# Kernel tuning notes

Hardware: AMD Instinct MI355X
Metric: run time of the kernel (lower is better)

The kernel has to match this reference:

```python
import jax, jax.numpy as jnp
import numpy as np
from jax import lax

EPS = 1e-5
DN = ('NCDHW', 'OIDHW', 'NCDHW')


def _instance_norm(x, w, b):
    # normalize over spatial dims per (batch, channel); biased variance like torch
    mu = jnp.mean(x, axis=(2, 3, 4), keepdims=True)
    var = jnp.mean((x - mu) ** 2, axis=(2, 3, 4), keepdims=True)
    xn = (x - mu) * lax.rsqrt(var + EPS)
    return xn * w[None, :, None, None, None] + b[None, :, None, None, None]


def _conv1x1(x, w, b):
    # w: [Cout, Cin]
    y = jnp.einsum('bcdhw,oc->bodhw', x, w)
    return y + b[None, :, None, None, None]


def _dwconv3(x, w, b):
    # depthwise 3x3x3, padding 1; w: [C, 1, 3, 3, 3]
    y = lax.conv_general_dilated(x, w, (1, 1, 1), 'SAME',
                                 dimension_numbers=DN,
                                 feature_group_count=w.shape[0])
    return y + b[None, :, None, None, None]


def setup_inputs() -> dict:
    key = jax.random.key(0)
    ks = jax.random.split(key, 8)
    C, half = 64, 32
    B, D, H, W = 1, 96, 96, 96
    s1 = 1.0 / np.sqrt(C)          # fan_in of 1x1 conv
    s3 = 1.0 / np.sqrt(27.0)       # fan_in of depthwise 3x3x3
    return {
        'x': jax.random.normal(ks[0], (B, C, D, H, W), jnp.float32),
        'norm_w': jnp.ones((C,), jnp.float32),
        'norm_b': jnp.zeros((C,), jnp.float32),
        'in_proj_w': jax.random.normal(ks[1], (C, C), jnp.float32) * s1,
        'in_proj_b': jnp.zeros((C,), jnp.float32),
        'conv_ssm_w': jax.random.normal(ks[2], (half, 1, 3, 3, 3), jnp.float32) * s3,
        'conv_ssm_b': jnp.zeros((half,), jnp.float32),
        'mamba_w': jax.random.normal(ks[3], (half, 1, 3, 3, 3), jnp.float32) * s3,
        'mamba_b': jnp.zeros((half,), jnp.float32),
        'conv_sym_w': jax.random.normal(ks[4], (half, 1, 3, 3, 3), jnp.float32) * s3,
        'conv_sym_b': jnp.zeros((half,), jnp.float32),
        'out_proj_w': jax.random.normal(ks[5], (C, C), jnp.float32) * s1,
        'out_proj_b': jnp.zeros((C,), jnp.float32),
    }


def reference(x, norm_w, norm_b, in_proj_w, in_proj_b,
              conv_ssm_w, conv_ssm_b, mamba_w, mamba_b,
              conv_sym_w, conv_sym_b, out_proj_w, out_proj_b):
    residual = x
    xp = _conv1x1(_instance_norm(x, norm_w, norm_b), in_proj_w, in_proj_b)
    half = xp.shape[1] // 2
    x1, x2 = xp[:, :half], xp[:, half:]
    # SSM branch (TriDirectionalMamba fallback = depthwise conv3)
    x1 = _dwconv3(jax.nn.silu(_dwconv3(x1, conv_ssm_w, conv_ssm_b)), mamba_w, mamba_b)
    # symmetric conv branch
    x2 = jax.nn.silu(_dwconv3(x2, conv_sym_w, conv_sym_b))
    y = _conv1x1(jnp.concatenate([x1, x2], axis=1), out_proj_w, out_proj_b)
    return y + residual
```

## Files before the change

kernel.cpp:

```cpp
#include <hip/hip_runtime.h>

typedef unsigned short u16;
typedef unsigned int u32;
typedef short bf16x8 __attribute__((ext_vector_type(8)));
typedef float f32x16 __attribute__((ext_vector_type(16)));
typedef u16 u16x8 __attribute__((ext_vector_type(8)));

#define DIM 96
#define PLANE (DIM*DIM)
#define S 884736
#define C 64
#define HALF 32
#define PARTS 16
#define EPS 1e-5f
#define DSPLIT 4
#define DCHUNK (DIM/DSPLIT)

#define MFMA32(a,b,c) __builtin_amdgcn_mfma_f32_32x32x16_bf16(a,b,c,0,0,0)

__device__ __forceinline__ u16 f2bf(float f) {
  u32 u = __builtin_bit_cast(u32, f);
  return (u16)((u + 0x7FFFu + ((u >> 16) & 1u)) >> 16);
}
__device__ __forceinline__ float bf2f(u16 h) {
  return __builtin_bit_cast(float, (u32)h << 16);
}
__device__ __forceinline__ u32 cvt_pk_bf16(float lo, float hi) {
  u32 r;
  asm("v_cvt_pk_bf16_f32 %0, %1, %2" : "=v"(r) : "v"(lo), "v"(hi));
  return r;
}
__device__ __forceinline__ float silu(float v) { return v / (1.f + __expf(-v)); }
__device__ __forceinline__ u16x8 zero8() {
  u16x8 z;
  #pragma unroll
  for (int i = 0; i < 8; ++i) z[i] = 0;
  return z;
}

__global__ __launch_bounds__(256) void k1_stats(const float* __restrict__ x,
                                                u16* __restrict__ xb,
                                                float* __restrict__ psum,
                                                float* __restrict__ psq) {
  const int bid = blockIdx.x;
  const int ch = bid / PARTS, part = bid % PARTS;
  const int chunk = S / PARTS;
  const size_t base = (size_t)ch * S + (size_t)part * chunk;
  const float4* p = (const float4*)(x + base);
  ushort4* xb4 = (ushort4*)(xb + base);
  const int n4 = chunk / 4;
  float s = 0.f, q = 0.f;
  for (int i = threadIdx.x; i < n4; i += 256) {
    float4 v = p[i];
    s += (v.x + v.y) + (v.z + v.w);
    q += (v.x * v.x + v.y * v.y) + (v.z * v.z + v.w * v.w);
    union { u32 u[2]; ushort4 v4; } o;
    o.u[0] = cvt_pk_bf16(v.x, v.y);
    o.u[1] = cvt_pk_bf16(v.z, v.w);
    xb4[i] = o.v4;
  }
  #pragma unroll
  for (int off = 32; off > 0; off >>= 1) {
    s += __shfl_down(s, off);
    q += __shfl_down(q, off);
  }
  __shared__ float ls[4], lq[4];
  const int wid = threadIdx.x >> 6, lane = threadIdx.x & 63;
  if (lane == 0) { ls[wid] = s; lq[wid] = q; }
  __syncthreads();
  if (threadIdx.x == 0) {
    psum[bid] = (ls[0] + ls[1]) + (ls[2] + ls[3]);
    psq[bid]  = (lq[0] + lq[1]) + (lq[2] + lq[3]);
  }
}

__global__ __launch_bounds__(64) void k1b_prep(const float* __restrict__ psum,
    const float* __restrict__ psq,
    const float* __restrict__ norm_w, const float* __restrict__ norm_b,
    const float* __restrict__ in_w, const float* __restrict__ in_b,
    const float* __restrict__ out_w,
    u16* __restrict__ Wp, float* __restrict__ biasp, u16* __restrict__ Wo) {
  __shared__ float a_s[C], b2_s[C];
  const int t = threadIdx.x;
  float s = 0.f, q = 0.f;
  for (int i = 0; i < PARTS; ++i) { s += psum[t * PARTS + i]; q += psq[t * PARTS + i]; }
  const float inv = 1.f / (float)S;
  const float mu = s * inv;
  const float var = q * inv - mu * mu;
  const float rsig = rsqrtf(var + EPS);
  const float a = norm_w[t] * rsig;
  const float b2 = norm_b[t] - mu * a;
  a_s[t] = a; b2_s[t] = b2;
  __syncthreads();
  float bp = in_b[t];
  for (int c = 0; c < C; ++c) {
    const float w = in_w[t * C + c];
    Wp[t * C + c] = f2bf(w * a_s[c]);
    bp += b2_s[c] * w;
    Wo[t * C + c] = f2bf(out_w[t * C + c]);
  }
  biasp[t] = bp;
}

__global__ __launch_bounds__(256) void k2_mfma(const u16* __restrict__ xb,
    const u16* __restrict__ Wp, const float* __restrict__ biasp,
    u16* __restrict__ xp) {
  const int lane = threadIdx.x & 63, wid = threadIdx.x >> 6;
  const int n = lane & 31, hf = lane >> 5;
  const int v0 = blockIdx.x * 256 + wid * 64;
  bf16x8 A[2][4];
  #pragma unroll
  for (int t = 0; t < 2; ++t)
    #pragma unroll
    for (int s = 0; s < 4; ++s)
      A[t][s] = *(const bf16x8*)(Wp + (t * 32 + n) * C + s * 16 + hf * 8);

  f32x16 accE[2], accO[2];
  #pragma unroll
  for (int t = 0; t < 2; ++t)
    #pragma unroll
    for (int r = 0; r < 16; ++r) {
      const float b = biasp[t * 32 + (r & 3) + 8 * (r >> 2) + 4 * hf];
      accE[t][r] = b; accO[t][r] = b;
    }

  #pragma unroll
  for (int s = 0; s < 4; ++s) {
    union { u16 u[8]; bf16x8 v; } BE, BO;
    #pragma unroll
    for (int j = 0; j < 8; ++j) {
      const u32 xv = *(const u32*)(xb + (size_t)(s * 16 + hf * 8 + j) * S + v0 + 2 * n);
      BE.u[j] = (u16)(xv & 0xFFFFu); BO.u[j] = (u16)(xv >> 16);
    }
    #pragma unroll
    for (int t = 0; t < 2; ++t) {
      accE[t] = MFMA32(A[t][s], BE.v, accE[t]);
      accO[t] = MFMA32(A[t][s], BO.v, accO[t]);
    }
  }
  #pragma unroll
  for (int t = 0; t < 2; ++t)
    #pragma unroll
    for (int r = 0; r < 16; ++r) {
      const int o = t * 32 + (r & 3) + 8 * (r >> 2) + 4 * hf;
      *(u32*)(xp + (size_t)o * S + v0 + 2 * n) = cvt_pk_bf16(accE[t][r], accO[t][r]);
    }
}

__device__ __forceinline__ void fma_row8(float* __restrict__ a,
    const float* __restrict__ r, float t0, float t1, float t2) {
  #pragma unroll
  for (int i = 0; i < 8; ++i) a[i] += t0 * r[i] + t1 * r[i + 1] + t2 * r[i + 2];
}

template<bool SILU>
__global__ __launch_bounds__(192) void dwconv(const u16* __restrict__ srcA,
    const float* __restrict__ kwA, const float* __restrict__ bA,
    u16* __restrict__ dstA,
    const float* __restrict__ kwB, const float* __restrict__ bB,
    u16* __restrict__ dstB) {
  const int c = blockIdx.z;
  const u16* src = srcA + (size_t)c * S;
  u16* dst; const float* kwp; float bias;
  if (c < HALF) { dst = dstA + (size_t)c * S;          kwp = kwA + c * 27;          bias = bA[c]; }
  else          { dst = dstB + (size_t)(c - HALF) * S; kwp = kwB + (c - HALF) * 27; bias = bB[c - HALF]; }
  float kw[27];
  #pragma unroll
  for (int i = 0; i < 27; ++i) kw[i] = kwp[i];

  const int w8 = threadIdx.x * 8;
  const int h  = blockIdx.x * 16 + threadIdx.y;
  const bool hm = h > 0, hp = h < DIM - 1;
  const bool wlo = w8 > 0, whi = w8 < DIM - 8;
  const int d0 = blockIdx.y * DCHUNK;

  u16x8 Qm[3]; u16 Qlo[3], Qhi[3];
  u16x8 Pm[3]; u16 Plo[3], Phi[3];
  float r0[10], r1[10], r2[10];
  float A[8], B[8], o8[8];

  #define RAWLOAD(M, LO, HI, PPTR) { \
    const u16* _p = (PPTR); \
    if (hm) { M[0] = *(const u16x8*)(_p - DIM); LO[0] = wlo ? _p[-DIM - 1] : (u16)0; HI[0] = whi ? _p[-DIM + 8] : (u16)0; } \
    else    { M[0] = zero8(); LO[0] = 0; HI[0] = 0; } \
    {         M[1] = *(const u16x8*)(_p);       LO[1] = wlo ? _p[-1]       : (u16)0; HI[1] = whi ? _p[8]        : (u16)0; } \
    if (hp) { M[2] = *(const u16x8*)(_p + DIM); LO[2] = wlo ? _p[DIM - 1]  : (u16)0; HI[2] = whi ? _p[DIM + 8]  : (u16)0; } \
    else    { M[2] = zero8(); LO[2] = 0; HI[2] = 0; } }

  #define CONVERT(M, LO, HI) { \
    r0[0] = bf2f(LO[0]); r1[0] = bf2f(LO[1]); r2[0] = bf2f(LO[2]); \
    _Pragma("unroll") \
    for (int i = 0; i < 8; ++i) { \
      r0[1 + i] = bf2f(M[0][i]); r1[1 + i] = bf2f(M[1][i]); r2[1 + i] = bf2f(M[2][i]); } \
    r0[9] = bf2f(HI[0]); r1[9] = bf2f(HI[1]); r2[9] = bf2f(HI[2]); }

  #define ZROWS() { \
    _Pragma("unroll") \
    for (int i = 0; i < 10; ++i) { r0[i] = 0.f; r1[i] = 0.f; r2[i] = 0.f; } }

  #define CBLK(ACC, K0) \
    fma_row8(ACC, r0, kw[(K0) + 0], kw[(K0) + 1], kw[(K0) + 2]); \
    fma_row8(ACC, r1, kw[(K0) + 3], kw[(K0) + 4], kw[(K0) + 5]); \
    fma_row8(ACC, r2, kw[(K0) + 6], kw[(K0) + 7], kw[(K0) + 8]);

  #define COMPUTE_STORE() { \
    _Pragma("unroll") \
    for (int i = 0; i < 8; ++i) o8[i] = A[i]; \
    CBLK(o8, 18); \
    _Pragma("unroll") \
    for (int i = 0; i < 8; ++i) A[i] = B[i]; \
    CBLK(A, 9); \
    _Pragma("unroll") \
    for (int i = 0; i < 8; ++i) B[i] = bias; \
    CBLK(B, 0); \
    if (SILU) { \
      _Pragma("unroll") \
      for (int i = 0; i < 8; ++i) o8[i] = silu(o8[i]); \
    } \
    union { u32 u[4]; u16x8 v; } _o; \
    _Pragma("unroll") \
    for (int i = 0; i < 4; ++i) _o.u[i] = cvt_pk_bf16(o8[2 * i], o8[2 * i + 1]); \
    *(u16x8*)db = _o.v; \
    db += PLANE; }

  const u16* pb0 = src + h * DIM + w8;

  if (d0 > 0) {
    RAWLOAD(Qm, Qlo, Qhi, pb0 + (size_t)(d0 - 1) * PLANE); CONVERT(Qm, Qlo, Qhi);
    #pragma unroll
    for (int i = 0; i < 8; ++i) B[i] = bias;
    CBLK(B, 0);
  } else {
    #pragma unroll
    for (int i = 0; i < 8; ++i) B[i] = bias;
  }
  RAWLOAD(Qm, Qlo, Qhi, pb0 + (size_t)d0 * PLANE); CONVERT(Qm, Qlo, Qhi);
  #pragma unroll
  for (int i = 0; i < 8; ++i) { A[i] = B[i]; B[i] = bias; }
  CBLK(A, 9);
  CBLK(B, 0);
  RAWLOAD(Qm, Qlo, Qhi, pb0 + (size_t)(d0 + 1) * PLANE);
  RAWLOAD(Pm, Plo, Phi, pb0 + (size_t)(d0 + 2) * PLANE);
  const u16* pA = pb0 + (size_t)(d0 + 3) * PLANE;
  const u16* pB = pA + PLANE;
  u16* db = dst + (size_t)d0 * PLANE + h * DIM + w8;

  #pragma unroll 1
  for (int d = d0; d < d0 + DCHUNK; d += 2) {
    CONVERT(Qm, Qlo, Qhi);
    if (d + 3 < DIM) { RAWLOAD(Qm, Qlo, Qhi, pA); }
    pA += 2 * PLANE;
    COMPUTE_STORE();
    if (d + 2 < DIM) { CONVERT(Pm, Plo, Phi); } else { ZROWS(); }
    if (d + 4 < DIM) { RAWLOAD(Pm, Plo, Phi, pB); }
    pB += 2 * PLANE;
    COMPUTE_STORE();
  }
  #undef COMPUTE_STORE
  #undef CBLK
  #undef ZROWS
  #undef CONVERT
  #undef RAWLOAD
}

__global__ __launch_bounds__(256) void k4b_mfma(const u16* __restrict__ z_lo,
    const u16* __restrict__ z_hi, const u16* __restrict__ xb,
    const u16* __restrict__ Wo, const float* __restrict__ ob,
    float* __restrict__ out) {
  const int lane = threadIdx.x & 63, wid = threadIdx.x >> 6;
  const int n = lane & 31, hf = lane >> 5;
  const int v0 = blockIdx.x * 256 + wid * 64;
  bf16x8 A[2][4];
  #pragma unroll
  for (int t = 0; t < 2; ++t)
    #pragma unroll
    for (int s = 0; s < 4; ++s)
      A[t][s] = *(const bf16x8*)(Wo + (t * 32 + n) * C + s * 16 + hf * 8);

  f32x16 accE[2], accO[2];
  #pragma unroll
  for (int t = 0; t < 2; ++t)
    #pragma unroll
    for (int r = 0; r < 16; ++r) {
      const float b = ob[t * 32 + (r & 3) + 8 * (r >> 2) + 4 * hf];
      accE[t][r] = b; accO[t][r] = b;
    }

  #pragma unroll
  for (int s = 0; s < 4; ++s) {
    const u16* zbase = (s < 2) ? z_lo + (size_t)(s * 16) * S
                               : z_hi + (size_t)((s - 2) * 16) * S;
    union { u16 u[8]; bf16x8 v; } BE, BO;
    #pragma unroll
    for (int j = 0; j < 8; ++j) {
      const u32 zv = *(const u32*)(zbase + (size_t)(hf * 8 + j) * S + v0 + 2 * n);
      BE.u[j] = (u16)(zv & 0xFFFFu); BO.u[j] = (u16)(zv >> 16);
    }
    #pragma unroll
    for (int t = 0; t < 2; ++t) {
      accE[t] = MFMA32(A[t][s], BE.v, accE[t]);
      accO[t] = MFMA32(A[t][s], BO.v, accO[t]);
    }
  }
  #pragma unroll
  for (int t = 0; t < 2; ++t)
    #pragma unroll
    for (int r = 0; r < 16; ++r) {
      const int o = t * 32 + (r & 3) + 8 * (r >> 2) + 4 * hf;
      const u32 xr = *(const u32*)(xb + (size_t)o * S + v0 + 2 * n);
      float2 ov;
      ov.x = accE[t][r] + bf2f((u16)(xr & 0xFFFFu));
      ov.y = accO[t][r] + bf2f((u16)(xr >> 16));
      *(float2*)(out + (size_t)o * S + v0 + 2 * n) = ov;
    }
}

extern "C" void kernel_launch(void* const* d_in, const int* in_sizes, int n_in,
                              void* d_out, int out_size, void* d_ws, size_t ws_size,
                              hipStream_t stream) {
  const float* x      = (const float*)d_in[0];
  const float* norm_w = (const float*)d_in[1];
  const float* norm_b = (const float*)d_in[2];
  const float* in_w   = (const float*)d_in[3];
  const float* in_b   = (const float*)d_in[4];
  const float* ssm_w  = (const float*)d_in[5];
  const float* ssm_b  = (const float*)d_in[6];
  const float* mam_w  = (const float*)d_in[7];
  const float* mam_b  = (const float*)d_in[8];
  const float* sym_w  = (const float*)d_in[9];
  const float* sym_b  = (const float*)d_in[10];
  const float* out_w  = (const float*)d_in[11];
  const float* out_b  = (const float*)d_in[12];
  float* out = (float*)d_out;

  u16* xb   = (u16*)d_ws;
  u16* xp   = xb + (size_t)C * S;
  u16* t1   = xp + (size_t)C * S;
  u16* z_hi = t1 + (size_t)HALF * S;
  u16* z_lo = xp;
  float* psum  = (float*)(z_hi + (size_t)HALF * S);
  float* psq   = psum + C * PARTS;
  u16* Wp      = (u16*)(psq + C * PARTS);
  u16* Wo      = Wp + C * C;
  float* biasp = (float*)(Wo + C * C);

  k1_stats<<<C * PARTS, 256, 0, stream>>>(x, xb, psum, psq);
  k1b_prep<<<1, 64, 0, stream>>>(psum, psq, norm_w, norm_b, in_w, in_b, out_w,
                                 Wp, biasp, Wo);
  k2_mfma<<<S / 256, 256, 0, stream>>>(xb, Wp, biasp, xp);
  dwconv<true><<<dim3(DIM / 16, DSPLIT, C), dim3(12, 16, 1), 0, stream>>>(
      xp, ssm_w, ssm_b, t1, sym_w, sym_b, z_hi);
  dwconv<false><<<dim3(DIM / 16, DSPLIT, HALF), dim3(12, 16, 1), 0, stream>>>(
      t1, mam_w, mam_b, z_lo, mam_w, mam_b, z_lo);
  k4b_mfma<<<S / 256, 256, 0, stream>>>(z_lo, z_hi, xb, Wo, out_b, out);
}
```

Baseline: 387.4 us.

## Stage depthwise conv input planes through double-buffered LDS with halo rows

The depthwise 3x3x3 conv kernel now cooperatively loads each 18-row halo tile of a depth plane into a double-buffered shared-memory ring with zero-padded borders. Each thread then reads its three rows and edge values from LDS instead of issuing per-thread global loads, including scalar halo loads. This removes redundant global traffic and the uncoalesced single-element edge loads. In exchange it adds a __syncthreads per depth step and shortens the global prefetch distance. The FMA inner loop is also split into explicit fmaf chains.

After: 354.1 us. -8.6%, faster.

```diff
diff --git a/kernel.cpp b/kernel.cpp
--- a/kernel.cpp
+++ b/kernel.cpp
@@ -15,6 +15,10 @@
 #define EPS 1e-5f
 #define DSPLIT 4
 #define DCHUNK (DIM/DSPLIT)
+
+#define RPAD 104
+#define LROWS 18
+#define LBUF (8 + LROWS*RPAD)
 
 #define MFMA32(a,b,c) __builtin_amdgcn_mfma_f32_32x32x16_bf16(a,b,c,0,0,0)
 
@@ -147,10 +151,14 @@
     }
 }
 
-__device__ __forceinline__ void fma_row8(float* __restrict__ a,
+__device__ __forceinline__ void fma3(float* __restrict__ a,
     const float* __restrict__ r, float t0, float t1, float t2) {
   #pragma unroll
-  for (int i = 0; i < 8; ++i) a[i] += t0 * r[i] + t1 * r[i + 1] + t2 * r[i + 2];
+  for (int i = 0; i < 8; ++i) a[i] = fmaf(t0, r[i], a[i]);
+  #pragma unroll
+  for (int i = 0; i < 8; ++i) a[i] = fmaf(t1, r[i + 1], a[i]);
+  #pragma unroll
+  for (int i = 0; i < 8; ++i) a[i] = fmaf(t2, r[i + 2], a[i]);
 }
 
 template<bool SILU>
@@ -159,6 +167,7 @@
     u16* __restrict__ dstA,
     const float* __restrict__ kwB, const float* __restrict__ bB,
     u16* __restrict__ dstB) {
+  __shared__ u16 lds[2][LBUF];
   const int c = blockIdx.z;
   const u16* src = srcA + (size_t)c * S;
   u16* dst; const float* kwp; float bias;
@@ -168,42 +177,82 @@
   #pragma unroll
   for (int i = 0; i < 27; ++i) kw[i] = kwp[i];
 
-  const int w8 = threadIdx.x * 8;
-  const int h  = blockIdx.x * 16 + threadIdx.y;
-  const bool hm = h > 0, hp = h < DIM - 1;
-  const bool wlo = w8 > 0, whi = w8 < DIM - 8;
+  const int tx = threadIdx.x, ty = threadIdx.y;
+  const int tid = ty * 12 + tx;
+  const int w8 = tx * 8;
+  const int h0 = blockIdx.x * 16;
   const int d0 = blockIdx.y * DCHUNK;
 
-  u16x8 Qm[3]; u16 Qlo[3], Qhi[3];
-  u16x8 Pm[3]; u16 Plo[3], Phi[3];
+  if (tid < 38) {
+    const int b = tid / 19, k = tid % 19;
+    *(u16x8*)&lds[b][RPAD * k] = zero8();
+  }
+
+  const int s_row0 = tid / 12, s_cc0 = tid % 12;
+  const int s_row1 = (192 + tid) / 12, s_cc1 = (192 + tid) % 12;
+  const bool has2 = tid < 24;
+  const int s_h0 = h0 - 1 + s_row0;
+  const int s_h1 = h0 - 1 + s_row1;
+  const bool h0ok = (unsigned)s_h0 < DIM;
+  const bool h1ok = has2 && ((unsigned)s_h1 < DIM);
+  u16x8 vs0, vs1;
+
+  #define STAGE_LOAD(DD) { \
+    vs0 = zero8(); vs1 = zero8(); \
+    if (((unsigned)(DD) < DIM) && h0ok) \
+      vs0 = *(const u16x8*)(src + (size_t)(DD) * PLANE + s_h0 * DIM + s_cc0 * 8); \
+    if (((unsigned)(DD) < DIM) && h1ok) \
+      vs1 = *(const u16x8*)(src + (size_t)(DD) * PLANE + s_h1 * DIM + s_cc1 * 8); }
+
+  #define STAGE_WRITE(WB) { \
+    *(u16x8*)&lds[WB][8 + s_row0 * RPAD + s_cc0 * 8] = vs0; \
+    if (has2) *(u16x8*)&lds[WB][8 + s_row1 * RPAD + s_cc1 * 8] = vs1; }
+
   float r0[10], r1[10], r2[10];
   float A[8], B[8], o8[8];
 
-  #define RAWLOAD(M, LO, HI, PPTR) { \
-    const u16* _p = (PPTR); \
-    if (hm) { M[0] = *(const u16x8*)(_p - DIM); LO[0] = wlo ? _p[-DIM - 1] : (u16)0; HI[0] = whi ? _p[-DIM + 8] : (u16)0; } \
-    else    { M[0] = zero8(); LO[0] = 0; HI[0] = 0; } \
-    {         M[1] = *(const u16x8*)(_p);       LO[1] = wlo ? _p[-1]       : (u16)0; HI[1] = whi ? _p[8]        : (u16)0; } \
-    if (hp) { M[2] = *(const u16x8*)(_p + DIM); LO[2] = wlo ? _p[DIM - 1]  : (u16)0; HI[2] = whi ? _p[DIM + 8]  : (u16)0; } \
-    else    { M[2] = zero8(); LO[2] = 0; HI[2] = 0; } }
-
-  #define CONVERT(M, LO, HI) { \
-    r0[0] = bf2f(LO[0]); r1[0] = bf2f(LO[1]); r2[0] = bf2f(LO[2]); \
-    _Pragma("unroll") \
-    for (int i = 0; i < 8; ++i) { \
-      r0[1 + i] = bf2f(M[0][i]); r1[1 + i] = bf2f(M[1][i]); r2[1 + i] = bf2f(M[2][i]); } \
-    r0[9] = bf2f(HI[0]); r1[9] = bf2f(HI[1]); r2[9] = bf2f(HI[2]); }
-
-  #define ZROWS() { \
-    _Pragma("unroll") \
-    for (int i = 0; i < 10; ++i) { r0[i] = 0.f; r1[i] = 0.f; r2[i] = 0.f; } }
-
-  #define CBLK(ACC, K0) \
-    fma_row8(ACC, r0, kw[(K0) + 0], kw[(K0) + 1], kw[(K0) + 2]); \
-    fma_row8(ACC, r1, kw[(K0) + 3], kw[(K0) + 4], kw[(K0) + 5]); \
-    fma_row8(ACC, r2, kw[(K0) + 6], kw[(K0) + 7], kw[(K0) + 8]);
-
-  #define COMPUTE_STORE() { \
+  #define LOADROW(R, ROWI, RB) { \
+    const u16* _lb = &lds[RB][8 + (ROWI) * RPAD + w8]; \
+    const u16x8 _m = *(const u16x8*)_lb; \
+    const u16 _lo = _lb[-1], _hi = _lb[8]; \
+    R[0] = bf2f(_lo); \
+    _Pragma("unroll") \
+    for (int i = 0; i < 8; ++i) R[1 + i] = bf2f(_m[i]); \
+    R[9] = bf2f(_hi); }
+
+  #define LOADROWS(RB) { LOADROW(r0, ty, RB); LOADROW(r1, ty + 1, RB); LOADROW(r2, ty + 2, RB); }
+
+  #define CBLK(ACC, K0) { \
+    fma3(ACC, r0, kw[(K0) + 0], kw[(K0) + 1], kw[(K0) + 2]); \
+    fma3(ACC, r1, kw[(K0) + 3], kw[(K0) + 4], kw[(K0) + 5]); \
+    fma3(ACC, r2, kw[(K0) + 6], kw[(K0) + 7], kw[(K0) + 8]); }
+
+  STAGE_LOAD(d0 - 1);
+  STAGE_WRITE(0);
+  __syncthreads();
+
+  LOADROWS(0);
+  STAGE_LOAD(d0);
+  #pragma unroll
+  for (int i = 0; i < 8; ++i) B[i] = bias;
+  CBLK(B, 0);
+  STAGE_WRITE(1);
+  __syncthreads();
+
+  LOADROWS(1);
+  STAGE_LOAD(d0 + 1);
+  #pragma unroll
+  for (int i = 0; i < 8; ++i) { A[i] = B[i]; B[i] = bias; }
+  CBLK(A, 9);
+  CBLK(B, 0);
+  STAGE_WRITE(0);
+  __syncthreads();
+
+  u16* db = dst + (size_t)d0 * PLANE + (size_t)(h0 + ty) * DIM + w8;
+
+  #define ROUND_BODY(D, RB, WB, DO_STG) { \
+    LOADROWS(RB); \
+    if (DO_STG) STAGE_LOAD((D) + 2); \
     _Pragma("unroll") \
     for (int i = 0; i < 8; ++i) o8[i] = A[i]; \
     CBLK(o8, 18); \
@@ -221,46 +270,21 @@
     _Pragma("unroll") \
     for (int i = 0; i < 4; ++i) _o.u[i] = cvt_pk_bf16(o8[2 * i], o8[2 * i + 1]); \
     *(u16x8*)db = _o.v; \
-    db += PLANE; }
-
-  const u16* pb0 = src + h * DIM + w8;
-
-  if (d0 > 0) {
-    RAWLOAD(Qm, Qlo, Qhi, pb0 + (size_t)(d0 - 1) * PLANE); CONVERT(Qm, Qlo, Qhi);
-    #pragma unroll
-    for (int i = 0; i < 8; ++i) B[i] = bias;
-    CBLK(B, 0);
-  } else {
-    #pragma unroll
-    for (int i = 0; i < 8; ++i) B[i] = bias;
-  }
-  RAWLOAD(Qm, Qlo, Qhi, pb0 + (size_t)d0 * PLANE); CONVERT(Qm, Qlo, Qhi);
-  #pragma unroll
-  for (int i = 0; i < 8; ++i) { A[i] = B[i]; B[i] = bias; }
-  CBLK(A, 9);
-  CBLK(B, 0);
-  RAWLOAD(Qm, Qlo, Qhi, pb0 + (size_t)(d0 + 1) * PLANE);
-  RAWLOAD(Pm, Plo, Phi, pb0 + (size_t)(d0 + 2) * PLANE);
-  const u16* pA = pb0 + (size_t)(d0 + 3) * PLANE;
-  const u16* pB = pA + PLANE;
-  u16* db = dst + (size_t)d0 * PLANE + h * DIM + w8;
+    db += PLANE; \
+    if (DO_STG) STAGE_WRITE(WB); \
+    __syncthreads(); }
 
   #pragma unroll 1
   for (int d = d0; d < d0 + DCHUNK; d += 2) {
-    CONVERT(Qm, Qlo, Qhi);
-    if (d + 3 < DIM) { RAWLOAD(Qm, Qlo, Qhi, pA); }
-    pA += 2 * PLANE;
-    COMPUTE_STORE();
-    if (d + 2 < DIM) { CONVERT(Pm, Plo, Phi); } else { ZROWS(); }
-    if (d + 4 < DIM) { RAWLOAD(Pm, Plo, Phi, pB); }
-    pB += 2 * PLANE;
-    COMPUTE_STORE();
-  }
-  #undef COMPUTE_STORE
+    ROUND_BODY(d, 0, 1, true);
+    ROUND_BODY(d + 1, 1, 0, (d + 2) < d0 + DCHUNK);
+  }
+  #undef ROUND_BODY
   #undef CBLK
-  #undef ZROWS
-  #undef CONVERT
-  #undef RAWLOAD
+  #undef LOADROWS
+  #undef LOADROW
+  #undef STAGE_WRITE
+  #undef STAGE_LOAD
 }
 
 __global__ __launch_bounds__(256) void k4b_mfma(const u16* __restrict__ z_lo,
```
